# Optimization experiments

Measured on AMD Instinct MI355X. Metric: run time of the kernel, lower is better.

## Reference

```python
import jax, jax.numpy as jnp
import numpy as np

B, D, E = 65536, 1024, 16
H1, H2 = 128, 64          # expert hidden dims (hidden_dim=128, hidden_dim//2)
R1, R2 = 64, 32           # router hidden dims
EPS = 1e-5                # BatchNorm eps


def setup_inputs() -> dict:
    key = jax.random.key(0)
    ks = jax.random.split(key, 16)
    s = 0.02
    inp = {
        "x": jax.random.normal(ks[0], (B, D), jnp.float32),
        # router BatchNorm1d (eval mode: running stats)
        "r_gamma": jnp.ones((D,), jnp.float32),
        "r_beta": jnp.zeros((D,), jnp.float32),
        "r_mean": jnp.zeros((D,), jnp.float32),
        "r_var": jnp.ones((D,), jnp.float32),
        # router MLP D->64->32->16
        "rW1": jax.random.normal(ks[1], (D, R1), jnp.float32) * s,
        "rb1": jnp.full((R1,), 0.1, jnp.float32),
        "rW2": jax.random.normal(ks[2], (R1, R2), jnp.float32) * s,
        "rb2": jnp.full((R2,), 0.1, jnp.float32),
        "rW3": jax.random.normal(ks[3], (R2, E), jnp.float32) * s,
        "rb3": jnp.full((E,), 0.1, jnp.float32),
        # per-expert BatchNorm1d (eval mode)
        "e_gamma": jnp.ones((E, D), jnp.float32),
        "e_beta": jnp.zeros((E, D), jnp.float32),
        "e_mean": jnp.zeros((E, D), jnp.float32),
        "e_var": jnp.ones((E, D), jnp.float32),
        # per-expert MLP D->128->64->1, stacked along expert dim
        "eW1": jax.random.normal(ks[4], (E, D, H1), jnp.float32) * s,
        "eb1": jnp.full((E, H1), 0.1, jnp.float32),
        "eW2": jax.random.normal(ks[5], (E, H1, H2), jnp.float32) * s,
        "eb2": jnp.full((E, H2), 0.1, jnp.float32),
        "eW3": jax.random.normal(ks[6], (E, H2, 1), jnp.float32) * s,
        "eb3": jnp.full((E, 1), 0.1, jnp.float32),
    }
    return inp


def reference(x, r_gamma, r_beta, r_mean, r_var, rW1, rb1, rW2, rb2, rW3, rb3,
              e_gamma, e_beta, e_mean, e_var, eW1, eb1, eW2, eb2, eW3, eb3):
    # ---- router: BN (eval) -> Linear/ReLU -> Linear/ReLU -> Linear -> softmax
    xn = (x - r_mean) * (r_gamma / jnp.sqrt(r_var + EPS)) + r_beta   # [B,D]
    h = jax.nn.relu(xn @ rW1 + rb1)
    h = jax.nn.relu(h @ rW2 + rb2)
    routing_weights = jax.nn.softmax(h @ rW3 + rb3, axis=1)          # [B,E]

    # ---- experts: fold per-expert BN into first linear to avoid [E,B,D] copy
    scale = e_gamma / jnp.sqrt(e_var + EPS)                          # [E,D]
    shift = e_beta - e_mean * scale                                  # [E,D]
    W1_eff = eW1 * scale[:, :, None]                                 # [E,D,H1]
    b1_eff = eb1 + jnp.einsum('ed,edh->eh', shift, eW1)              # [E,H1]

    h1 = jax.nn.relu(jnp.einsum('bd,edh->ebh', x, W1_eff) + b1_eff[:, None, :])  # [E,B,H1]
    h2 = jax.nn.relu(jnp.einsum('ebh,ehk->ebk', h1, eW2) + eb2[:, None, :])      # [E,B,H2]
    logits = jnp.einsum('ebk,eko->ebo', h2, eW3) + eb3[:, None, :]               # [E,B,1]
    expert_outputs = jax.nn.sigmoid(logits[:, :, 0]).T               # [B,E]

    weighted_pred = jnp.sum(routing_weights * expert_outputs, axis=1)  # [B]
    return weighted_pred, routing_weights, expert_outputs
```

## Files before the change

kernel.cpp:

```cpp
#include <hip/hip_runtime.h>


typedef unsigned short u16;
typedef __attribute__((ext_vector_type(8))) short bf16x8;
typedef __attribute__((ext_vector_type(4))) float f32x4;
typedef __attribute__((ext_vector_type(8))) unsigned short u16x8;
typedef __attribute__((ext_vector_type(4))) unsigned short u16x4;

#define MFMA16(a, b, c) __builtin_amdgcn_mfma_f32_16x16x32_bf16(a, b, c, 0, 0, 0)

#define B_ROWS 65536
#define DIM 1024
#define NE 16
#define EPS 1e-5f

__device__ inline u16 f2bf(float f) {
    union { float f; unsigned u; } c; c.f = f;
    unsigned u = c.u;
    return (u16)((u + 0x7fffu + ((u >> 16) & 1u)) >> 16);
}

__device__ inline void gload16(const u16* g, u16* s) {
    __builtin_amdgcn_global_load_lds(
        (const __attribute__((address_space(1))) unsigned int*)g,
        (__attribute__((address_space(3))) unsigned int*)s,
        16, 0, 0);
}


__device__ void body_prep_x(int blk, int tid, const float* __restrict__ x,
                            u16* __restrict__ xs_g, u16* __restrict__ lds) {
    int p = tid & 15, rloc = tid >> 4;
    int r_g = blk * 16 + rloc;
    int r = r_g & 127;
    int lb = p & 7;
    int phys = lb ^ (r & 7);
    const float* xrow = x + (size_t)r_g * 1024;
#pragma unroll
    for (int i = 0; i < 8; ++i) {
        int kc = 2 * i + (p >> 3);
        int c = kc * 64 + lb * 8;
        float4 f0 = *(const float4*)(xrow + c);
        float4 f1 = *(const float4*)(xrow + c + 4);
        u16x8 u;
        u[0] = f2bf(f0.x); u[1] = f2bf(f0.y); u[2] = f2bf(f0.z); u[3] = f2bf(f0.w);
        u[4] = f2bf(f1.x); u[5] = f2bf(f1.y); u[6] = f2bf(f1.z); u[7] = f2bf(f1.w);
        *(u16x8*)&lds[(kc * 16 + rloc) * 64 + phys * 8] = u;
    }
    __syncthreads();
    int rb = blk >> 3, R0 = (blk & 7) * 16;
    int tl = tid & 127, th = tid >> 7;
#pragma unroll
    for (int jj = 0; jj < 8; ++jj) {
        int kc = 2 * jj + th;
        u16x8 v = *(const u16x8*)&lds[kc * 1024 + tl * 8];
        *(u16x8*)&xs_g[(((size_t)(rb * 16 + kc) * 128 + R0 + (tl >> 3)) << 6) + (tl & 7) * 8] = v;
    }
}

__device__ void body_prep_w1s(int t, const float* __restrict__ eW1, const float* __restrict__ eg,
                              const float* __restrict__ ev, u16* __restrict__ w1s) {
    int p = t & 7, r = (t >> 3) & 127, kc = (t >> 10) & 15, e = t >> 14;
    int lb = p ^ (r & 7);
    u16x8 u;
#pragma unroll
    for (int j = 0; j < 8; ++j) {
        int d = kc * 64 + lb * 8 + j;
        float sc = eg[e * 1024 + d] * rsqrtf(ev[e * 1024 + d] + EPS);
        u[j] = f2bf(eW1[((size_t)e * 1024 + d) * 128 + r] * sc);
    }
    *(u16x8*)&w1s[((size_t)((e * 16 + kc) * 128 + r) << 6) + p * 8] = u;
}

__device__ void body_prep_b1(int g, int lane, const float* __restrict__ eW1,
                             const float* __restrict__ eg, const float* __restrict__ eb,
                             const float* __restrict__ em, const float* __restrict__ ev,
                             const float* __restrict__ eb1, float* __restrict__ b1e) {
    int e = g >> 7, h = g & 127;
    float s = 0.f;
    for (int d = lane; d < 1024; d += 64) {
        float sc = eg[e * 1024 + d] * rsqrtf(ev[e * 1024 + d] + EPS);
        float sh = eb[e * 1024 + d] - em[e * 1024 + d] * sc;
        s += sh * eW1[((size_t)e * 1024 + d) * 128 + h];
    }
#pragma unroll
    for (int m = 1; m < 64; m <<= 1) s += __shfl_xor(s, m, 64);
    if (lane == 0) b1e[e * 128 + h] = eb1[e * 128 + h] + s;
}

__device__ void body_prep_rw1s(int t, const float* __restrict__ rW1, const float* __restrict__ rg,
                               const float* __restrict__ rv, u16* __restrict__ rw1s) {
    int p = t & 7, r = (t >> 3) & 63, kc = t >> 9;
    int lb = p ^ (r & 7);
    u16x8 u;
#pragma unroll
    for (int j = 0; j < 8; ++j) {
        int d = kc * 64 + lb * 8 + j;
        float sc = rg[d] * rsqrtf(rv[d] + EPS);
        u[j] = f2bf(rW1[d * 64 + r] * sc);
    }
    *(u16x8*)&rw1s[((kc * 64 + r) << 6) + p * 8] = u;
}

__device__ void body_prep_rb1(int j, int lane, const float* __restrict__ rW1,
                              const float* __restrict__ rg, const float* __restrict__ rbta,
                              const float* __restrict__ rm, const float* __restrict__ rv,
                              const float* __restrict__ rb1, float* __restrict__ rb1e) {
    float s = 0.f;
    for (int d = lane; d < 1024; d += 64) {
        float sc = rg[d] * rsqrtf(rv[d] + EPS);
        float sh = rbta[d] - rm[d] * sc;
        s += sh * rW1[d * 64 + j];
    }
#pragma unroll
    for (int m = 1; m < 64; m <<= 1) s += __shfl_xor(s, m, 64);
    if (lane == 0) rb1e[j] = rb1[j] + s;
}

__device__ void body_prep_w2s(int t, const float* __restrict__ eW2, u16* __restrict__ w2s) {
    int p = t & 15, j = (t >> 4) & 63, e = t >> 10;
    int lb = p ^ (j & 7);
    int h0 = lb * 8;
    u16x8 u;
#pragma unroll
    for (int jj = 0; jj < 8; ++jj)
        u[jj] = f2bf(eW2[((size_t)e * 128 + h0 + jj) * 64 + j]);
    *(u16x8*)&w2s[((e * 64 + j) << 7) + p * 8] = u;
}

__global__ __launch_bounds__(256) void prep_all(
    const float* __restrict__ x, u16* __restrict__ xs_g,
    const float* __restrict__ eW1, const float* __restrict__ eg,
    const float* __restrict__ eb, const float* __restrict__ em,
    const float* __restrict__ ev, const float* __restrict__ eb1,
    u16* __restrict__ w1s, float* __restrict__ b1e,
    const float* __restrict__ rW1, const float* __restrict__ rg,
    const float* __restrict__ rbta, const float* __restrict__ rm,
    const float* __restrict__ rv, const float* __restrict__ rb1,
    u16* __restrict__ rw1s, float* __restrict__ rb1e,
    const float* __restrict__ eW2, u16* __restrict__ w2s) {
    __shared__ __align__(16) u16 lds[16384];
    int bid = blockIdx.x, tid = threadIdx.x;
    if (bid < 4096) {
        body_prep_x(bid, tid, x, xs_g, lds);
    } else if (bid < 5120) {
        body_prep_w1s((bid - 4096) * 256 + tid, eW1, eg, ev, w1s);
    } else if (bid < 5632) {
        body_prep_b1((bid - 5120) * 4 + (tid >> 6), tid & 63, eW1, eg, eb, em, ev, eb1, b1e);
    } else if (bid < 5664) {
        body_prep_rw1s((bid - 5632) * 256 + tid, rW1, rg, rv, rw1s);
    } else if (bid < 5680) {
        body_prep_rb1((bid - 5664) * 4 + (tid >> 6), tid & 63, rW1, rg, rbta, rm, rv, rb1, rb1e);
    } else {
        body_prep_w2s((bid - 5680) * 256 + tid, eW2, w2s);
    }
}

__global__ __launch_bounds__(256) void fused_main(
    const u16* __restrict__ xs_g, const u16* __restrict__ w1s,
    const float* __restrict__ b1e, const u16* __restrict__ w2s,
    const float* __restrict__ eb2, const float* __restrict__ eW3,
    const float* __restrict__ eb3, float* __restrict__ out_eo,
    const u16* __restrict__ rw1s, const float* __restrict__ rb1e,
    const float* __restrict__ rW2, const float* __restrict__ rb2,
    const float* __restrict__ rW3, const float* __restrict__ rb3,
    float* __restrict__ out_rw) {
    __shared__ __align__(16) char smem[53248];

    int tid = threadIdx.x;
    int wave = tid >> 6, lane = tid & 63;
    int quad = lane >> 4, l15 = lane & 15;

    if (blockIdx.x >= 512) {
        u16* sA = (u16*)smem;
        u16* sW2 = (u16*)(smem + 32768);
        int bid = blockIdx.x - 512;
        int e = bid & 15, rb = bid >> 4;
        int wm = wave & 1, wn = wave >> 1;

        f32x4 acc[4][4] = {};
        const u16* xg_base = xs_g + (size_t)rb * 131072;
        const u16* wg_base = w1s + (size_t)e * 131072;

        for (int kc = 0; kc < 16; ++kc) {
            const u16* xg = xg_base + kc * 8192;
            const u16* wg = wg_base + kc * 8192;
            int so = wave * 2048;
#pragma unroll
            for (int i = 0; i < 4; ++i) {
                gload16(xg + so + i * 512 + lane * 8, &sA[so + i * 512]);
                gload16(wg + so + i * 512 + lane * 8, &sA[8192 + so + i * 512]);
            }
            __syncthreads();
#pragma unroll
            for (int ks = 0; ks < 2; ++ks) {
                bf16x8 af[4], bfr[4];
#pragma unroll
                for (int s = 0; s < 4; ++s) {
                    int h = wm * 64 + s * 16 + l15;
                    int phys = (ks * 4 + quad) ^ (h & 7);
                    af[s] = *(const bf16x8*)&sA[8192 + h * 64 + phys * 8];
                }
#pragma unroll
                for (int t = 0; t < 4; ++t) {
                    int m = wn * 64 + t * 16 + l15;
                    int phys = (ks * 4 + quad) ^ (m & 7);
                    bfr[t] = *(const bf16x8*)&sA[m * 64 + phys * 8];
                }
#pragma unroll
                for (int s = 0; s < 4; ++s)
#pragma unroll
                    for (int t = 0; t < 4; ++t)
                        acc[s][t] = MFMA16(af[s], bfr[t], acc[s][t]);
            }
            __syncthreads();
        }

        {
            const u16* wg2 = w2s + e * 8192;
            int so = wave * 2048;
#pragma unroll
            for (int i = 0; i < 4; ++i)
                gload16(wg2 + so + i * 512 + lane * 8, &sW2[so + i * 512]);
        }
#pragma unroll
        for (int s = 0; s < 4; ++s) {
            int h0 = wm * 64 + s * 16 + quad * 4;
            float4 bv = *(const float4*)&b1e[e * 128 + h0];
            float bva[4] = {bv.x, bv.y, bv.z, bv.w};
#pragma unroll
            for (int t = 0; t < 4; ++t) {
                int m = wn * 64 + t * 16 + l15;
                u16x4 pk;
#pragma unroll
                for (int r = 0; r < 4; ++r) {
                    float v = acc[s][t][r] + bva[r];
                    pk[r] = f2bf(fmaxf(v, 0.f));
                }
                int phys = (h0 >> 3) ^ (m & 7);
                *(u16x4*)&sA[m * 128 + phys * 8 + (h0 & 7)] = pk;
            }
        }
        __syncthreads();

        f32x4 acc2[2][4] = {};
#pragma unroll
        for (int ks = 0; ks < 4; ++ks) {
            bf16x8 a2[2], b2[4];
#pragma unroll
            for (int s = 0; s < 2; ++s) {
                int m = wave * 32 + s * 16 + l15;
                int phys = (ks * 4 + quad) ^ (m & 7);
                a2[s] = *(const bf16x8*)&sA[m * 128 + phys * 8];
            }
#pragma unroll
            for (int t = 0; t < 4; ++t) {
                int j = t * 16 + l15;
                int phys = (ks * 4 + quad) ^ (j & 7);
                b2[t] = *(const bf16x8*)&sW2[j * 128 + phys * 8];
            }
#pragma unroll
            for (int s = 0; s < 2; ++s)
#pragma unroll
                for (int t = 0; t < 4; ++t)
                    acc2[s][t] = MFMA16(a2[s], b2[t], acc2[s][t]);
        }

        float b2v[4], w3v[4];
#pragma unroll
        for (int t = 0; t < 4; ++t) {
            int j = t * 16 + l15;
            b2v[t] = eb2[e * 64 + j];
            w3v[t] = eW3[e * 64 + j];
        }
        float be3 = eb3[e];
#pragma unroll
        for (int s = 0; s < 2; ++s) {
            float sv[4] = {0.f, 0.f, 0.f, 0.f};
#pragma unroll
            for (int t = 0; t < 4; ++t)
#pragma unroll
                for (int r = 0; r < 4; ++r) {
                    float v = acc2[s][t][r] + b2v[t];
                    sv[r] += fmaxf(v, 0.f) * w3v[t];
                }
#pragma unroll
            for (int mask = 1; mask < 16; mask <<= 1)
#pragma unroll
                for (int r = 0; r < 4; ++r) sv[r] += __shfl_xor(sv[r], mask, 64);
            if (l15 == 0) {
#pragma unroll
                for (int r = 0; r < 4; ++r) {
                    int m = wave * 32 + s * 16 + quad * 4 + r;
                    float z = sv[r] + be3;
                    out_eo[(size_t)(rb * 128 + m) * 16 + e] = 1.f / (1.f + __expf(-z));
                }
            }
        }
    } else {
        char* region0 = smem;
        float* h2s = (float*)(smem + 34816);
        u16* xs_l = (u16*)region0;
        u16* rw_l = (u16*)(region0 + 16384);
        float* h_r = (float*)region0;
        int rb = blockIdx.x;

        f32x4 acc[4][2] = {};
        const u16* xg_base = xs_g + (size_t)rb * 131072;

        for (int kc = 0; kc < 16; ++kc) {
            const u16* xg = xg_base + kc * 8192;
            const u16* rg = rw1s + kc * 4096;
            int so = wave * 2048;
#pragma unroll
            for (int i = 0; i < 4; ++i)
                gload16(xg + so + i * 512 + lane * 8, &xs_l[so + i * 512]);
            int so2 = wave * 1024;
#pragma unroll
            for (int i = 0; i < 2; ++i)
                gload16(rg + so2 + i * 512 + lane * 8, &rw_l[so2 + i * 512]);
            __syncthreads();
#pragma unroll
            for (int ks = 0; ks < 2; ++ks) {
                bf16x8 af[4], bfr[2];
#pragma unroll
                for (int s = 0; s < 4; ++s) {
                    int j = s * 16 + l15;
                    int phys = (ks * 4 + quad) ^ (j & 7);
                    af[s] = *(const bf16x8*)&rw_l[j * 64 + phys * 8];
                }
#pragma unroll
                for (int t = 0; t < 2; ++t) {
                    int m = wave * 32 + t * 16 + l15;
                    int phys = (ks * 4 + quad) ^ (m & 7);
                    bfr[t] = *(const bf16x8*)&xs_l[m * 64 + phys * 8];
                }
#pragma unroll
                for (int s = 0; s < 4; ++s)
#pragma unroll
                    for (int t = 0; t < 2; ++t)
                        acc[s][t] = MFMA16(af[s], bfr[t], acc[s][t]);
            }
            __syncthreads();
        }

#pragma unroll
        for (int s = 0; s < 4; ++s) {
            int j0 = s * 16 + quad * 4;
            float4 bv = *(const float4*)&rb1e[j0];
#pragma unroll
            for (int t = 0; t < 2; ++t) {
                int m = wave * 32 + t * 16 + l15;
                float4 hv;
                hv.x = fmaxf(acc[s][t][0] + bv.x, 0.f);
                hv.y = fmaxf(acc[s][t][1] + bv.y, 0.f);
                hv.z = fmaxf(acc[s][t][2] + bv.z, 0.f);
                hv.w = fmaxf(acc[s][t][3] + bv.w, 0.f);
                *(float4*)&h_r[m * 68 + j0] = hv;
            }
        }
        __syncthreads();

        {
            int m = tid & 127, qg = tid >> 7;
            float h2r[16];
#pragma unroll
            for (int k = 0; k < 16; ++k) h2r[k] = 0.f;
            for (int i = 0; i < 64; ++i) {
                float hv = h_r[m * 68 + i];
                const float4* wrow = (const float4*)&rW2[i * 32 + qg * 16];
                float w[16];
                *(float4*)&w[0] = wrow[0];
                *(float4*)&w[4] = wrow[1];
                *(float4*)&w[8] = wrow[2];
                *(float4*)&w[12] = wrow[3];
#pragma unroll
                for (int k = 0; k < 16; ++k) h2r[k] += hv * w[k];
            }
#pragma unroll
            for (int k = 0; k < 16; ++k)
                h2r[k] = fmaxf(h2r[k] + rb2[qg * 16 + k], 0.f);
#pragma unroll
            for (int k = 0; k < 16; k += 4)
                *(float4*)&h2s[m * 36 + qg * 16 + k] = *(float4*)&h2r[k];
        }
        __syncthreads();

        if (tid < 128) {
            int mm = tid;
            float lg[16];
#pragma unroll
            for (int o = 0; o < 16; ++o) lg[o] = 0.f;
            for (int q = 0; q < 32; ++q) {
                float hv = h2s[mm * 36 + q];
                const float4* wr = (const float4*)&rW3[q * 16];
                float w[16];
                *(float4*)&w[0] = wr[0];
                *(float4*)&w[4] = wr[1];
                *(float4*)&w[8] = wr[2];
                *(float4*)&w[12] = wr[3];
#pragma unroll
                for (int o = 0; o < 16; ++o) lg[o] += hv * w[o];
            }
#pragma unroll
            for (int o = 0; o < 16; ++o) lg[o] += rb3[o];
            float mx = lg[0];
#pragma unroll
            for (int o = 1; o < 16; ++o) mx = fmaxf(mx, lg[o]);
            float ss = 0.f;
#pragma unroll
            for (int o = 0; o < 16; ++o) { lg[o] = __expf(lg[o] - mx); ss += lg[o]; }
            float inv = 1.f / ss;
            size_t base = (size_t)(rb * 128 + mm) * 16;
#pragma unroll
            for (int o = 0; o < 16; o += 4) {
                float4 v;
                v.x = lg[o] * inv; v.y = lg[o + 1] * inv;
                v.z = lg[o + 2] * inv; v.w = lg[o + 3] * inv;
                *(float4*)&out_rw[base + o] = v;
            }
        }
    }
}

__global__ void combine_kernel(const float* __restrict__ rw, const float* __restrict__ eo,
                               float* __restrict__ wp) {
    int b = blockIdx.x * 256 + threadIdx.x;
    const float4* r4 = (const float4*)(rw + (size_t)b * 16);
    const float4* o4 = (const float4*)(eo + (size_t)b * 16);
    float s = 0.f;
#pragma unroll
    for (int k = 0; k < 4; ++k) {
        float4 r = r4[k], o = o4[k];
        s += r.x * o.x + r.y * o.y + r.z * o.z + r.w * o.w;
    }
    wp[b] = s;
}


extern "C" void kernel_launch(void* const* d_in, const int* in_sizes, int n_in,
                              void* d_out, int out_size, void* d_ws, size_t ws_size,
                              hipStream_t stream) {
    const float* x       = (const float*)d_in[0];
    const float* r_gamma = (const float*)d_in[1];
    const float* r_beta  = (const float*)d_in[2];
    const float* r_mean  = (const float*)d_in[3];
    const float* r_var   = (const float*)d_in[4];
    const float* rW1     = (const float*)d_in[5];
    const float* rb1     = (const float*)d_in[6];
    const float* rW2     = (const float*)d_in[7];
    const float* rb2     = (const float*)d_in[8];
    const float* rW3     = (const float*)d_in[9];
    const float* rb3     = (const float*)d_in[10];
    const float* e_gamma = (const float*)d_in[11];
    const float* e_beta  = (const float*)d_in[12];
    const float* e_mean  = (const float*)d_in[13];
    const float* e_var   = (const float*)d_in[14];
    const float* eW1     = (const float*)d_in[15];
    const float* eb1     = (const float*)d_in[16];
    const float* eW2     = (const float*)d_in[17];
    const float* eb2     = (const float*)d_in[18];
    const float* eW3     = (const float*)d_in[19];
    const float* eb3     = (const float*)d_in[20];

    char* ws = (char*)d_ws;
    u16* xs_g   = (u16*)ws;
    u16* w1s    = (u16*)(ws + 134217728);
    u16* rw1s   = (u16*)(ws + 138412032);
    u16* w2s    = (u16*)(ws + 138543104);
    float* b1e  = (float*)(ws + 138805248);
    float* rb1e = (float*)(ws + 138813440);

    float* out_wp = (float*)d_out;
    float* out_rw = out_wp + B_ROWS;
    float* out_eo = out_rw + (size_t)B_ROWS * NE;

    prep_all<<<5744, 256, 0, stream>>>(
        x, xs_g,
        eW1, e_gamma, e_beta, e_mean, e_var, eb1, w1s, b1e,
        rW1, r_gamma, r_beta, r_mean, r_var, rb1, rw1s, rb1e,
        eW2, w2s);

    fused_main<<<8704, 256, 0, stream>>>(
        xs_g, w1s, b1e, w2s, eb2, eW3, eb3, out_eo,
        rw1s, rb1e, rW2, rb2, rW3, rb3, out_rw);

    combine_kernel<<<256, 256, 0, stream>>>(out_rw, out_eo, out_wp);
}
```

Measured before the change: 777.2 us.

## Retile expert GEMM to 256x256 blocks with a 4-stage LDS ring pipeline

Rewrites the main fused kernel so each 512-thread block computes two experts (256 hidden cols) against 256 rows, with K tiled at 32 and a 4-deep LDS ring buffer using global_load_lds, vmcnt waits and raw barriers to overlap loads with MFMA. The prep kernels change layouts to match the new 32-wide K tiles and swizzle, and W2 fragments are now read straight from global into registers. The intent is to raise arithmetic intensity by reusing each x tile across two experts, and to hide memory latency. The cost is much higher register and LDS pressure (128KB smem, launch bounds 512x2), which may limit occupancy.

```diff
diff --git a/kernel.cpp b/kernel.cpp
--- a/kernel.cpp
+++ b/kernel.cpp
@@ -10,9 +10,15 @@
 #define MFMA16(a, b, c) __builtin_amdgcn_mfma_f32_16x16x32_bf16(a, b, c, 0, 0, 0)
 
 #define B_ROWS 65536
-#define DIM 1024
 #define NE 16
 #define EPS 1e-5f
+
+#define SBAR() __builtin_amdgcn_s_barrier()
+#define VMCNT(n)                                             \
+    do {                                                     \
+        asm volatile("s_waitcnt vmcnt(" #n ")" ::: "memory");\
+        __builtin_amdgcn_sched_barrier(0);                   \
+    } while (0)
 
 __device__ inline u16 f2bf(float f) {
     union { float f; unsigned u; } c; c.f = f;
@@ -32,9 +38,8 @@
                             u16* __restrict__ xs_g, u16* __restrict__ lds) {
     int p = tid & 15, rloc = tid >> 4;
     int r_g = blk * 16 + rloc;
-    int r = r_g & 127;
     int lb = p & 7;
-    int phys = lb ^ (r & 7);
+    int swz = (rloc >> 1) & 3;
     const float* xrow = x + (size_t)r_g * 1024;
 #pragma unroll
     for (int i = 0; i < 8; ++i) {
@@ -45,31 +50,35 @@
         u16x8 u;
         u[0] = f2bf(f0.x); u[1] = f2bf(f0.y); u[2] = f2bf(f0.z); u[3] = f2bf(f0.w);
         u[4] = f2bf(f1.x); u[5] = f2bf(f1.y); u[6] = f2bf(f1.z); u[7] = f2bf(f1.w);
-        *(u16x8*)&lds[(kc * 16 + rloc) * 64 + phys * 8] = u;
+        int s = c >> 5;
+        int q = (c >> 3) & 3;
+        *(u16x8*)&lds[s * 512 + rloc * 32 + ((q ^ swz) << 3)] = u;
     }
     __syncthreads();
-    int rb = blk >> 3, R0 = (blk & 7) * 16;
-    int tl = tid & 127, th = tid >> 7;
-#pragma unroll
-    for (int jj = 0; jj < 8; ++jj) {
-        int kc = 2 * jj + th;
-        u16x8 v = *(const u16x8*)&lds[kc * 1024 + tl * 8];
-        *(u16x8*)&xs_g[(((size_t)(rb * 16 + kc) * 128 + R0 + (tl >> 3)) << 6) + (tl & 7) * 8] = v;
+    int rb = blk >> 4, m0 = (blk & 15) * 16;
+    int lane = tid & 63, th = tid >> 6;
+#pragma unroll
+    for (int j = 0; j < 8; ++j) {
+        int c = j * 4 + th;
+        u16x8 v = *(const u16x8*)&lds[c * 512 + lane * 8];
+        *(u16x8*)&xs_g[((size_t)(rb * 32 + c) << 13) + m0 * 32 + lane * 8] = v;
     }
 }
 
 __device__ void body_prep_w1s(int t, const float* __restrict__ eW1, const float* __restrict__ eg,
                               const float* __restrict__ ev, u16* __restrict__ w1s) {
-    int p = t & 7, r = (t >> 3) & 127, kc = (t >> 10) & 15, e = t >> 14;
-    int lb = p ^ (r & 7);
+    int qp = t & 3, h = (t >> 2) & 255, s = (t >> 10) & 31, nt = t >> 15;
+    int q = qp ^ ((h >> 1) & 3);
+    int e = nt * 2 + (h >> 7), hl = h & 127;
+    int k0 = s * 32 + q * 8;
     u16x8 u;
 #pragma unroll
     for (int j = 0; j < 8; ++j) {
-        int d = kc * 64 + lb * 8 + j;
+        int d = k0 + j;
         float sc = eg[e * 1024 + d] * rsqrtf(ev[e * 1024 + d] + EPS);
-        u[j] = f2bf(eW1[((size_t)e * 1024 + d) * 128 + r] * sc);
-    }
-    *(u16x8*)&w1s[((size_t)((e * 16 + kc) * 128 + r) << 6) + p * 8] = u;
+        u[j] = f2bf(eW1[((size_t)e * 1024 + d) * 128 + hl] * sc);
+    }
+    *(u16x8*)&w1s[((size_t)(nt * 32 + s) << 13) + h * 32 + qp * 8] = u;
 }
 
 __device__ void body_prep_b1(int g, int lane, const float* __restrict__ eW1,
@@ -90,16 +99,17 @@
 
 __device__ void body_prep_rw1s(int t, const float* __restrict__ rW1, const float* __restrict__ rg,
                                const float* __restrict__ rv, u16* __restrict__ rw1s) {
-    int p = t & 7, r = (t >> 3) & 63, kc = t >> 9;
-    int lb = p ^ (r & 7);
+    int qp = t & 3, jj = (t >> 2) & 63, s = t >> 8;
+    int q = qp ^ ((jj >> 1) & 3);
+    int k0 = s * 32 + q * 8;
     u16x8 u;
 #pragma unroll
-    for (int j = 0; j < 8; ++j) {
-        int d = kc * 64 + lb * 8 + j;
+    for (int k = 0; k < 8; ++k) {
+        int d = k0 + k;
         float sc = rg[d] * rsqrtf(rv[d] + EPS);
-        u[j] = f2bf(rW1[d * 64 + r] * sc);
-    }
-    *(u16x8*)&rw1s[((kc * 64 + r) << 6) + p * 8] = u;
+        u[k] = f2bf(rW1[d * 64 + jj] * sc);
+    }
+    *(u16x8*)&rw1s[(s << 11) + jj * 32 + qp * 8] = u;
 }
 
 __device__ void body_prep_rb1(int j, int lane, const float* __restrict__ rW1,
@@ -156,7 +166,7 @@
     }
 }
 
-__global__ __launch_bounds__(256) void fused_main(
+__global__ __launch_bounds__(512, 2) void fused_main(
     const u16* __restrict__ xs_g, const u16* __restrict__ w1s,
     const float* __restrict__ b1e, const u16* __restrict__ w2s,
     const float* __restrict__ eb2, const float* __restrict__ eW3,
@@ -165,125 +175,133 @@
     const float* __restrict__ rW2, const float* __restrict__ rb2,
     const float* __restrict__ rW3, const float* __restrict__ rb3,
     float* __restrict__ out_rw) {
-    __shared__ __align__(16) char smem[53248];
+    __shared__ __align__(16) char smem[131072];
 
     int tid = threadIdx.x;
-    int wave = tid >> 6, lane = tid & 63;
-    int quad = lane >> 4, l15 = lane & 15;
-
-    if (blockIdx.x >= 512) {
-        u16* sA = (u16*)smem;
-        u16* sW2 = (u16*)(smem + 32768);
-        int bid = blockIdx.x - 512;
-        int e = bid & 15, rb = bid >> 4;
-        int wm = wave & 1, wn = wave >> 1;
-
-        f32x4 acc[4][4] = {};
-        const u16* xg_base = xs_g + (size_t)rb * 131072;
-        const u16* wg_base = w1s + (size_t)e * 131072;
-
-        for (int kc = 0; kc < 16; ++kc) {
-            const u16* xg = xg_base + kc * 8192;
-            const u16* wg = wg_base + kc * 8192;
-            int so = wave * 2048;
-#pragma unroll
-            for (int i = 0; i < 4; ++i) {
-                gload16(xg + so + i * 512 + lane * 8, &sA[so + i * 512]);
-                gload16(wg + so + i * 512 + lane * 8, &sA[8192 + so + i * 512]);
-            }
-            __syncthreads();
-#pragma unroll
-            for (int ks = 0; ks < 2; ++ks) {
-                bf16x8 af[4], bfr[4];
-#pragma unroll
-                for (int s = 0; s < 4; ++s) {
-                    int h = wm * 64 + s * 16 + l15;
-                    int phys = (ks * 4 + quad) ^ (h & 7);
-                    af[s] = *(const bf16x8*)&sA[8192 + h * 64 + phys * 8];
-                }
-#pragma unroll
-                for (int t = 0; t < 4; ++t) {
-                    int m = wn * 64 + t * 16 + l15;
-                    int phys = (ks * 4 + quad) ^ (m & 7);
-                    bfr[t] = *(const bf16x8*)&sA[m * 64 + phys * 8];
-                }
-#pragma unroll
-                for (int s = 0; s < 4; ++s)
-#pragma unroll
-                    for (int t = 0; t < 4; ++t)
-                        acc[s][t] = MFMA16(af[s], bfr[t], acc[s][t]);
-            }
-            __syncthreads();
-        }
-
-        {
-            const u16* wg2 = w2s + e * 8192;
-            int so = wave * 2048;
-#pragma unroll
-            for (int i = 0; i < 4; ++i)
-                gload16(wg2 + so + i * 512 + lane * 8, &sW2[so + i * 512]);
-        }
-#pragma unroll
-        for (int s = 0; s < 4; ++s) {
-            int h0 = wm * 64 + s * 16 + quad * 4;
-            float4 bv = *(const float4*)&b1e[e * 128 + h0];
+    int wave = tid >> 6, lane = tid & 63, quad = lane >> 4, l15 = lane & 15;
+    int phq = (quad ^ ((l15 >> 1) & 3)) * 8;
+
+    if (blockIdx.x >= 256) {
+        int i = blockIdx.x - 256;
+        int rb = (i & 7) * 32 + ((i >> 3) >> 3);
+        int nt = (i >> 3) & 7;
+        int wm = wave >> 2, wn = wave & 3;
+
+        u16* ring = (u16*)smem;
+        const u16* gA = w1s + ((size_t)nt << 18);
+        const u16* gB = xs_g + ((size_t)rb << 18);
+
+        f32x4 acc[8][4] = {};
+
+        auto STAGE = [&](int t) {
+            u16* ls = ring + (t & 3) * 16384 + wave * 1024;
+            const u16* ga = gA + (t << 13) + wave * 1024;
+            const u16* gb = gB + (t << 13) + wave * 1024;
+            gload16(ga + lane * 8, ls);
+            gload16(ga + 512 + lane * 8, ls + 512);
+            gload16(gb + lane * 8, ls + 8192);
+            gload16(gb + 512 + lane * 8, ls + 8192 + 512);
+        };
+        auto COMPUTE = [&](int t) {
+            const u16* lA = ring + (t & 3) * 16384;
+            const u16* lB = lA + 8192;
+            bf16x8 a[8], b[4];
+#pragma unroll
+            for (int ii = 0; ii < 8; ++ii)
+                a[ii] = *(const bf16x8*)&lA[(wm * 128 + ii * 16 + l15) * 32 + phq];
+#pragma unroll
+            for (int jj = 0; jj < 4; ++jj)
+                b[jj] = *(const bf16x8*)&lB[(wn * 64 + jj * 16 + l15) * 32 + phq];
+            __builtin_amdgcn_s_setprio(1);
+#pragma unroll
+            for (int ii = 0; ii < 8; ++ii)
+#pragma unroll
+                for (int jj = 0; jj < 4; ++jj)
+                    acc[ii][jj] = MFMA16(a[ii], b[jj], acc[ii][jj]);
+            __builtin_amdgcn_s_setprio(0);
+        };
+
+        STAGE(0); STAGE(1); STAGE(2);
+#pragma clang loop unroll(disable)
+        for (int s = 0; s < 29; ++s) {
+            SBAR();
+            STAGE(s + 3);
+            VMCNT(12);
+            SBAR();
+            COMPUTE(s);
+        }
+        SBAR(); VMCNT(8); SBAR(); COMPUTE(29);
+        SBAR(); VMCNT(4); SBAR(); COMPUTE(30);
+        SBAR(); VMCNT(0); SBAR(); COMPUTE(31);
+
+        int e = nt * 2 + wm;
+        u16* h1 = ring;
+        SBAR();
+#pragma unroll
+        for (int ii = 0; ii < 8; ++ii) {
+            float4 bv = *(const float4*)&b1e[e * 128 + ii * 16 + quad * 4];
             float bva[4] = {bv.x, bv.y, bv.z, bv.w};
-#pragma unroll
-            for (int t = 0; t < 4; ++t) {
-                int m = wn * 64 + t * 16 + l15;
+            int h0 = wm * 128 + ii * 16 + quad * 4;
+            int oc = h0 >> 3, hin = h0 & 7;
+#pragma unroll
+            for (int jj = 0; jj < 4; ++jj) {
+                int m = wn * 64 + jj * 16 + l15;
                 u16x4 pk;
 #pragma unroll
-                for (int r = 0; r < 4; ++r) {
-                    float v = acc[s][t][r] + bva[r];
-                    pk[r] = f2bf(fmaxf(v, 0.f));
-                }
-                int phys = (h0 >> 3) ^ (m & 7);
-                *(u16x4*)&sA[m * 128 + phys * 8 + (h0 & 7)] = pk;
-            }
-        }
-        __syncthreads();
-
-        f32x4 acc2[2][4] = {};
+                for (int r = 0; r < 4; ++r)
+                    pk[r] = f2bf(fmaxf(acc[ii][jj][r] + bva[r], 0.f));
+                int poc = (oc & 24) | ((oc ^ m) & 7);
+                *(u16x4*)&h1[m * 256 + poc * 8 + hin] = pk;
+            }
+        }
+        bf16x8 w2f[4][4];
+        const u16* gW2 = w2s + e * 8192;
+#pragma unroll
+        for (int ks = 0; ks < 4; ++ks)
+#pragma unroll
+            for (int tj = 0; tj < 4; ++tj) {
+                int jc = tj * 16 + l15;
+                int pq = (ks * 4 + quad) ^ (jc & 7);
+                w2f[ks][tj] = *(const bf16x8*)&gW2[jc * 128 + pq * 8];
+            }
+        asm volatile("s_waitcnt lgkmcnt(0)" ::: "memory");
+        __builtin_amdgcn_sched_barrier(0);
+        SBAR();
+
+        f32x4 acc2[4][4] = {};
 #pragma unroll
         for (int ks = 0; ks < 4; ++ks) {
-            bf16x8 a2[2], b2[4];
-#pragma unroll
-            for (int s = 0; s < 2; ++s) {
-                int m = wave * 32 + s * 16 + l15;
-                int phys = (ks * 4 + quad) ^ (m & 7);
-                a2[s] = *(const bf16x8*)&sA[m * 128 + phys * 8];
-            }
-#pragma unroll
-            for (int t = 0; t < 4; ++t) {
-                int j = t * 16 + l15;
-                int phys = (ks * 4 + quad) ^ (j & 7);
-                b2[t] = *(const bf16x8*)&sW2[j * 128 + phys * 8];
-            }
-#pragma unroll
-            for (int s = 0; s < 2; ++s)
-#pragma unroll
-                for (int t = 0; t < 4; ++t)
-                    acc2[s][t] = MFMA16(a2[s], b2[t], acc2[s][t]);
+            bf16x8 a2[4];
+#pragma unroll
+            for (int mi = 0; mi < 4; ++mi) {
+                int m = wn * 64 + mi * 16 + l15;
+                int oc2 = wm * 16 + ks * 4 + quad;
+                int poc2 = (oc2 & 24) | ((oc2 ^ m) & 7);
+                a2[mi] = *(const bf16x8*)&h1[m * 256 + poc2 * 8];
+            }
+#pragma unroll
+            for (int mi = 0; mi < 4; ++mi)
+#pragma unroll
+                for (int tj = 0; tj < 4; ++tj)
+                    acc2[mi][tj] = MFMA16(a2[mi], w2f[ks][tj], acc2[mi][tj]);
         }
 
         float b2v[4], w3v[4];
 #pragma unroll
-        for (int t = 0; t < 4; ++t) {
-            int j = t * 16 + l15;
-            b2v[t] = eb2[e * 64 + j];
-            w3v[t] = eW3[e * 64 + j];
+        for (int tj = 0; tj < 4; ++tj) {
+            int jc = tj * 16 + l15;
+            b2v[tj] = eb2[e * 64 + jc];
+            w3v[tj] = eW3[e * 64 + jc];
         }
         float be3 = eb3[e];
 #pragma unroll
-        for (int s = 0; s < 2; ++s) {
+        for (int mi = 0; mi < 4; ++mi) {
             float sv[4] = {0.f, 0.f, 0.f, 0.f};
 #pragma unroll
-            for (int t = 0; t < 4; ++t)
-#pragma unroll
-                for (int r = 0; r < 4; ++r) {
-                    float v = acc2[s][t][r] + b2v[t];
-                    sv[r] += fmaxf(v, 0.f) * w3v[t];
-                }
+            for (int tj = 0; tj < 4; ++tj)
+#pragma unroll
+                for (int r = 0; r < 4; ++r)
+                    sv[r] += fmaxf(acc2[mi][tj][r] + b2v[tj], 0.f) * w3v[tj];
 #pragma unroll
             for (int mask = 1; mask < 16; mask <<= 1)
 #pragma unroll
@@ -291,84 +309,74 @@
             if (l15 == 0) {
 #pragma unroll
                 for (int r = 0; r < 4; ++r) {
-                    int m = wave * 32 + s * 16 + quad * 4 + r;
+                    int m = wn * 64 + mi * 16 + quad * 4 + r;
                     float z = sv[r] + be3;
-                    out_eo[(size_t)(rb * 128 + m) * 16 + e] = 1.f / (1.f + __expf(-z));
+                    out_eo[(size_t)(rb * 256 + m) * 16 + e] = 1.f / (1.f + __expf(-z));
                 }
             }
         }
     } else {
-        char* region0 = smem;
-        float* h2s = (float*)(smem + 34816);
-        u16* xs_l = (u16*)region0;
-        u16* rw_l = (u16*)(region0 + 16384);
-        float* h_r = (float*)region0;
         int rb = blockIdx.x;
-
-        f32x4 acc[4][2] = {};
-        const u16* xg_base = xs_g + (size_t)rb * 131072;
-
-        for (int kc = 0; kc < 16; ++kc) {
-            const u16* xg = xg_base + kc * 8192;
-            const u16* rg = rw1s + kc * 4096;
-            int so = wave * 2048;
-#pragma unroll
-            for (int i = 0; i < 4; ++i)
-                gload16(xg + so + i * 512 + lane * 8, &xs_l[so + i * 512]);
-            int so2 = wave * 1024;
-#pragma unroll
-            for (int i = 0; i < 2; ++i)
-                gload16(rg + so2 + i * 512 + lane * 8, &rw_l[so2 + i * 512]);
+        u16* ldsX = (u16*)smem;
+        u16* ldsW = (u16*)smem + 16384;
+        float* h_r = (float*)smem;
+        float* h2s = (float*)(smem + 69632);
+        const u16* gB = xs_g + ((size_t)rb << 18);
+
+        f32x4 accr[4][2] = {};
+        for (int kt = 0; kt < 16; ++kt) {
+            const u16* gx = gB + ((size_t)(2 * kt) << 13) + wave * 1024;
+            const u16* gw = rw1s + ((2 * kt) << 11) + wave * 512;
+            u16* lx = ldsX + wave * 1024;
+            gload16(gx + lane * 8, lx);
+            gload16(gx + 512 + lane * 8, lx + 512);
+            gload16(gx + 8192 + lane * 8, lx + 8192);
+            gload16(gx + 8192 + 512 + lane * 8, lx + 8192 + 512);
+            gload16(gw + lane * 8, ldsW + wave * 512);
             __syncthreads();
 #pragma unroll
-            for (int ks = 0; ks < 2; ++ks) {
-                bf16x8 af[4], bfr[2];
-#pragma unroll
-                for (int s = 0; s < 4; ++s) {
-                    int j = s * 16 + l15;
-                    int phys = (ks * 4 + quad) ^ (j & 7);
-                    af[s] = *(const bf16x8*)&rw_l[j * 64 + phys * 8];
-                }
-#pragma unroll
-                for (int t = 0; t < 2; ++t) {
-                    int m = wave * 32 + t * 16 + l15;
-                    int phys = (ks * 4 + quad) ^ (m & 7);
-                    bfr[t] = *(const bf16x8*)&xs_l[m * 64 + phys * 8];
-                }
-#pragma unroll
-                for (int s = 0; s < 4; ++s)
-#pragma unroll
-                    for (int t = 0; t < 2; ++t)
-                        acc[s][t] = MFMA16(af[s], bfr[t], acc[s][t]);
+            for (int st = 0; st < 2; ++st) {
+                bf16x8 aw[4], bx[2];
+#pragma unroll
+                for (int jf = 0; jf < 4; ++jf)
+                    aw[jf] = *(const bf16x8*)&ldsW[st * 2048 + (jf * 16 + l15) * 32 + phq];
+#pragma unroll
+                for (int mf = 0; mf < 2; ++mf)
+                    bx[mf] = *(const bf16x8*)&ldsX[st * 8192 + (wave * 32 + mf * 16 + l15) * 32 + phq];
+#pragma unroll
+                for (int jf = 0; jf < 4; ++jf)
+#pragma unroll
+                    for (int mf = 0; mf < 2; ++mf)
+                        accr[jf][mf] = MFMA16(aw[jf], bx[mf], accr[jf][mf]);
             }
             __syncthreads();
         }
 
 #pragma unroll
-        for (int s = 0; s < 4; ++s) {
-            int j0 = s * 16 + quad * 4;
+        for (int jf = 0; jf < 4; ++jf) {
+            int j0 = jf * 16 + quad * 4;
             float4 bv = *(const float4*)&rb1e[j0];
 #pragma unroll
-            for (int t = 0; t < 2; ++t) {
-                int m = wave * 32 + t * 16 + l15;
+            for (int mf = 0; mf < 2; ++mf) {
+                int m = wave * 32 + mf * 16 + l15;
                 float4 hv;
-                hv.x = fmaxf(acc[s][t][0] + bv.x, 0.f);
-                hv.y = fmaxf(acc[s][t][1] + bv.y, 0.f);
-                hv.z = fmaxf(acc[s][t][2] + bv.z, 0.f);
-                hv.w = fmaxf(acc[s][t][3] + bv.w, 0.f);
+                hv.x = fmaxf(accr[jf][mf][0] + bv.x, 0.f);
+                hv.y = fmaxf(accr[jf][mf][1] + bv.y, 0.f);
+                hv.z = fmaxf(accr[jf][mf][2] + bv.z, 0.f);
+                hv.w = fmaxf(accr[jf][mf][3] + bv.w, 0.f);
                 *(float4*)&h_r[m * 68 + j0] = hv;
             }
         }
         __syncthreads();
 
         {
-            int m = tid & 127, qg = tid >> 7;
+            int m = tid & 255, qg = tid >> 8;
             float h2r[16];
 #pragma unroll
             for (int k = 0; k < 16; ++k) h2r[k] = 0.f;
-            for (int i = 0; i < 64; ++i) {
-                float hv = h_r[m * 68 + i];
-                const float4* wrow = (const float4*)&rW2[i * 32 + qg * 16];
+            for (int i2 = 0; i2 < 64; ++i2) {
+                float hv = h_r[m * 68 + i2];
+                const float4* wrow = (const float4*)&rW2[i2 * 32 + qg * 16];
                 float w[16];
                 *(float4*)&w[0] = wrow[0];
                 *(float4*)&w[4] = wrow[1];
@@ -386,7 +394,7 @@
         }
         __syncthreads();
 
-        if (tid < 128) {
+        if (tid < 256) {
             int mm = tid;
             float lg[16];
 #pragma unroll
@@ -411,7 +419,7 @@
 #pragma unroll
             for (int o = 0; o < 16; ++o) { lg[o] = __expf(lg[o] - mx); ss += lg[o]; }
             float inv = 1.f / ss;
-            size_t base = (size_t)(rb * 128 + mm) * 16;
+            size_t base = (size_t)(rb * 256 + mm) * 16;
 #pragma unroll
             for (int o = 0; o < 16; o += 4) {
                 float4 v;
@@ -481,7 +489,7 @@
         rW1, r_gamma, r_beta, r_mean, r_var, rb1, rw1s, rb1e,
         eW2, w2s);
 
-    fused_main<<<8704, 256, 0, stream>>>(
+    fused_main<<<2304, 512, 0, stream>>>(
         xs_g, w1s, b1e, w2s, eb2, eW3, eb3, out_eo,
         rw1s, rb1e, rW2, rb2, rW3, rb3, out_rw);
 
```

After: 731.3 us. 5.9% less time.
